# Optimization experiments

Measured on AMD Instinct MI355X. Metric: run time of the kernel, lower is better.

## Reference

```python
import jax, jax.numpy as jnp
import numpy as np
from jax import lax

DG = 8  # deformable groups


def conv3(x, w, b):
    # 3x3 stride-1 SAME conv, NCHW/OIHW
    y = lax.conv_general_dilated(x, w, (1, 1), 'SAME',
                                 dimension_numbers=('NCHW', 'OIHW', 'NCHW'))
    return y + b[None, :, None, None]


def lrelu(x):
    return jnp.where(x >= 0, x, 0.1 * x)


def _mdcn(x, offset, mask, w, b, dg):
    """Modulated deformable conv v2: 3x3, stride 1, pad 1, dilation 1, groups 1.
    offset: [B, 2*dg*9, H, W] (first dg*9 = y offsets, second dg*9 = x offsets),
    mask:   [B, dg*9, H, W] (already sigmoided)."""
    B, C, H, W = x.shape
    kk = 9
    Cg = C // dg
    off = offset.reshape(B, 2, dg, kk, H, W)
    oy, ox = off[:, 0], off[:, 1]            # [B, dg, kk, H, W]
    m = mask.reshape(B, dg, kk, H, W)
    ky = (jnp.arange(kk) // 3 - 1).astype(x.dtype).reshape(1, 1, kk, 1, 1)
    kx = (jnp.arange(kk) % 3 - 1).astype(x.dtype).reshape(1, 1, kk, 1, 1)
    hg = jnp.arange(H, dtype=x.dtype).reshape(1, 1, 1, H, 1)
    wg = jnp.arange(W, dtype=x.dtype).reshape(1, 1, 1, 1, W)
    py = hg + ky + oy                        # sampling positions (pad=1 cancels k-1 shift)
    px = wg + kx + ox
    y0 = jnp.floor(py)
    x0 = jnp.floor(px)
    wy = py - y0
    wx = px - x0
    xg = x.reshape(B, dg, Cg, H * W)
    acc = jnp.zeros((B, dg, Cg, kk, H, W), x.dtype)
    for dy, dx, wgt in ((0.0, 0.0, (1 - wy) * (1 - wx)),
                        (0.0, 1.0, (1 - wy) * wx),
                        (1.0, 0.0, wy * (1 - wx)),
                        (1.0, 1.0, wy * wx)):
        yy = y0 + dy
        xx = x0 + dx
        valid = (yy >= 0) & (yy < H) & (xx >= 0) & (xx < W)
        yi = jnp.clip(yy, 0, H - 1).astype(jnp.int32)
        xi = jnp.clip(xx, 0, W - 1).astype(jnp.int32)
        idx = (yi * W + xi).reshape(B, dg, 1, kk * H * W)
        v = jnp.take_along_axis(xg, idx, axis=3).reshape(B, dg, Cg, kk, H, W)
        acc = acc + v * (wgt * valid.astype(x.dtype))[:, :, None]
    acc = acc * m[:, :, None]                # modulation mask
    sampled = acc.reshape(B, C, kk, H, W)
    out = jnp.einsum('bckhw,ock->bohw', sampled, w.reshape(w.shape[0], C, kk))
    return out + b[None, :, None, None]


def _dcn_pack(x, feat, w_om, b_om, w, b):
    out = conv3(feat, w_om, b_om)            # [B, 3*dg*9, H, W]
    o1, o2, mr = jnp.split(out, 3, axis=1)
    offset = jnp.concatenate([o1, o2], axis=1)
    mask = jax.nn.sigmoid(mr)
    return _mdcn(x, offset, mask, w, b, DG)


def _forward(ref, neb,
             w_oc1, b_oc1, w_om1, b_om1, w_dcn1, b_dcn1, w_fc, b_fc,
             w_cas1, b_cas1, w_cas2, b_cas2, w_om2, b_om2, w_dcn2, b_dcn2,
             w_ta1, b_ta1, w_ta2, b_ta2, w_ff, b_ff):
    start = ref
    # --- PCD alignment (nbr_feat_l = neb, ref_feat_l = ref) ---
    off = lrelu(conv3(jnp.concatenate([neb, ref], axis=1), w_oc1, b_oc1))
    feat = _dcn_pack(neb, off, w_om1, b_om1, w_dcn1, b_dcn1)
    feat = lrelu(conv3(feat, w_fc, b_fc))
    off = jnp.concatenate([feat, ref], axis=1)
    off = lrelu(conv3(lrelu(conv3(off, w_cas1, b_cas1)), w_cas2, b_cas2))
    feat = lrelu(_dcn_pack(feat, off, w_om2, b_om2, w_dcn2, b_dcn2))
    # --- TSA fusion (ref=ref, neb=feat) ---
    emb_ref = conv3(ref, w_ta1, b_ta1)
    emb = conv3(feat, w_ta2, b_ta2)
    corr = jnp.sum(emb * emb_ref, axis=1, keepdims=True)  # [B,1,H,W]
    feat = lrelu(conv3(ref * corr, w_ff, b_ff))
    return feat + start


def setup_inputs() -> dict:
    key = jax.random.key(0)
    ks = jax.random.split(key, 32)
    B, C, H, W = 4, 64, 180, 320
    s = 0.05
    p = lambda k, shape: (jax.random.normal(k, shape, jnp.float32) * s)
    OM = 3 * DG * 9  # 216
    return {
        'ref': jax.random.normal(ks[0], (B, C, H, W), jnp.float32),
        'neb': jax.random.normal(ks[1], (B, C, H, W), jnp.float32),
        'w_oc1': p(ks[2], (C, 2 * C, 3, 3)), 'b_oc1': p(ks[3], (C,)),
        'w_om1': p(ks[4], (OM, C, 3, 3)),    'b_om1': p(ks[5], (OM,)),
        'w_dcn1': p(ks[6], (C, C, 3, 3)),    'b_dcn1': p(ks[7], (C,)),
        'w_fc': p(ks[8], (C, C, 3, 3)),      'b_fc': p(ks[9], (C,)),
        'w_cas1': p(ks[10], (C, 2 * C, 3, 3)), 'b_cas1': p(ks[11], (C,)),
        'w_cas2': p(ks[12], (C, C, 3, 3)),   'b_cas2': p(ks[13], (C,)),
        'w_om2': p(ks[14], (OM, C, 3, 3)),   'b_om2': p(ks[15], (OM,)),
        'w_dcn2': p(ks[16], (C, C, 3, 3)),   'b_dcn2': p(ks[17], (C,)),
        'w_ta1': p(ks[18], (C, C, 3, 3)),    'b_ta1': p(ks[19], (C,)),
        'w_ta2': p(ks[20], (C, C, 3, 3)),    'b_ta2': p(ks[21], (C,)),
        'w_ff': p(ks[22], (C, C, 3, 3)),     'b_ff': p(ks[23], (C,)),
    }


def reference(ref, neb,
              w_oc1, b_oc1, w_om1, b_om1, w_dcn1, b_dcn1, w_fc, b_fc,
              w_cas1, b_cas1, w_cas2, b_cas2, w_om2, b_om2, w_dcn2, b_dcn2,
              w_ta1, b_ta1, w_ta2, b_ta2, w_ff, b_ff):
    return _forward(ref, neb,
                    w_oc1, b_oc1, w_om1, b_om1, w_dcn1, b_dcn1, w_fc, b_fc,
                    w_cas1, b_cas1, w_cas2, b_cas2, w_om2, b_om2, w_dcn2, b_dcn2,
                    w_ta1, b_ta1, w_ta2, b_ta2, w_ff, b_ff)
```

## Files before the change

kernel.cpp:

```cpp
#include <hip/hip_runtime.h>
#include <cmath>


using short8 = __attribute__((ext_vector_type(8))) short;
using f32x4  = __attribute__((ext_vector_type(4))) float;

#define DEVINL static __device__ __forceinline__

DEVINL unsigned short f2bf(float f){
    unsigned u = __float_as_uint(f);
    u += 0x7fffu + ((u >> 16) & 1u);
    return (unsigned short)(u >> 16);
}
DEVINL unsigned pack2(float a, float b){ return (unsigned)f2bf(a) | ((unsigned)f2bf(b) << 16); }
DEVINL float bflo(unsigned u){ return __uint_as_float(u << 16); }
DEVINL float bfhi(unsigned u){ return __uint_as_float(u & 0xffff0000u); }
DEVINL float bf2f(unsigned short u){ return __uint_as_float((unsigned)u << 16); }
DEVINL float lrelu_f(float v){ return v >= 0.f ? v : 0.1f * v; }

__global__ __launch_bounds__(256) void nchw2nhwc2(const float* __restrict__ inA,
                                                  const float* __restrict__ inB,
                                                  unsigned short* __restrict__ outA,
                                                  unsigned short* __restrict__ outB)
{
    constexpr int HW = 180 * 320;
    const int blk = blockIdx.x;
    const float* in = (blk < 900) ? inA : inB;
    unsigned short* out = (blk < 900) ? outA : outB;
    size_t idx = (size_t)(blk % 900) * 256 + threadIdx.x;
    size_t bb = idx / HW, p = idx % HW;
    const float* src = in + (bb * 64) * (size_t)HW + p;
    unsigned short* dst = out + idx * 64;
    #pragma unroll
    for (int c0 = 0; c0 < 64; c0 += 16) {
        unsigned r[8];
        #pragma unroll
        for (int q = 0; q < 8; ++q)
            r[q] = pack2(src[(size_t)(c0 + 2*q) * HW], src[(size_t)(c0 + 2*q + 1) * HW]);
        *(uint4*)(dst + c0)     = *(uint4*)&r[0];
        *(uint4*)(dst + c0 + 8) = *(uint4*)&r[4];
    }
}

struct PrepArgs {
    const float* src[11];
    unsigned short* dst[11];
    int cout[11]; int cin[11]; int nch[11]; int kind[11];
};

__global__ __launch_bounds__(256) void prep_all(PrepArgs a)
{
    const int t = blockIdx.y;
    const int idx = blockIdx.x * 256 + threadIdx.x;
    if (a.kind[t] == 1) {
        if (idx >= 36864) return;
        int kk = idx & 31, oc = (idx >> 5) & 63, s = idx >> 11;
        int k = s * 32 + kk;
        int gt = k >> 3, c8 = k & 7;
        int g = gt / 9, tp = gt - g * 9;
        a.dst[t][idx] = f2bf(a.src[t][((size_t)oc * 64 + g * 8 + c8) * 9 + tp]);
    } else {
        int cin = a.cin[t], cout = a.cout[t];
        int ncs = cin / 32;
        int total = a.nch[t] * 9 * ncs * 2048;
        if (idx >= total) return;
        int kk = idx & 31, oc_l = (idx >> 5) & 63, rest = idx >> 11;
        int cs = rest % ncs; int rest2 = rest / ncs;
        int j = rest2 % 9; int ch = rest2 / 9;
        int oc = ch * 64 + oc_l, c = cs * 32 + kk;
        float v = (oc < cout) ? a.src[t][((size_t)oc * cin + c) * 9 + j] : 0.f;
        a.dst[t][idx] = f2bf(v);
    }
}

template<int CIN, bool TWO_IN, bool ACT, bool SCALE, int OUTMODE>
__global__ __launch_bounds__(256, (CIN == 128 ? 2 : 3)) void conv_mfma(
    const unsigned short* __restrict__ in0, const unsigned short* __restrict__ in1,
    const unsigned short* __restrict__ wgt, const float* __restrict__ bias,
    unsigned short* __restrict__ out, const float* __restrict__ corr,
    const float* __restrict__ res, float* __restrict__ outf, int COUT)
{
    constexpr int H = 180, W = 320, HW = H * W;
    constexpr int NCB = CIN / 8;
    constexpr int NCS = CIN / 32;
    __shared__ __align__(16) unsigned char lds[6 * 34 * CIN * 2];

    const int tid = threadIdx.x;
    const int b  = (OUTMODE == 1) ? 0 : blockIdx.z;
    const int ch = (OUTMODE == 1) ? blockIdx.z : 0;
    const int x0 = blockIdx.x * 32, y0 = blockIdx.y * 4;

    for (int t = tid; t < 6 * 34 * NCB; t += 256) {
        int cb = t % NCB; int r = t / NCB;
        int xp = r % 34, yp = r / 34;
        int gx = x0 - 1 + xp, gy = y0 - 1 + yp;
        uint4 v = make_uint4(0, 0, 0, 0);
        if (gx >= 0 && gx < W && gy >= 0 && gy < H) {
            size_t pix = (size_t)b * HW + (size_t)gy * W + gx;
            const unsigned short* src;
            if (TWO_IN) src = (cb < 8) ? (in0 + pix * 64 + cb * 8) : (in1 + pix * 64 + (cb - 8) * 8);
            else        src = in0 + pix * CIN + cb * 8;
            v = *(const uint4*)src;
            if (SCALE) {
                float cv = corr[pix];
                v.x = pack2(bflo(v.x) * cv, bfhi(v.x) * cv);
                v.y = pack2(bflo(v.y) * cv, bfhi(v.y) * cv);
                v.z = pack2(bflo(v.z) * cv, bfhi(v.z) * cv);
                v.w = pack2(bflo(v.w) * cv, bfhi(v.w) * cv);
            }
        }
        int blk = cb ^ (xp & 7);
        *(uint4*)&lds[(size_t)((yp * 34 + xp) * NCB + blk) * 16] = v;
    }
    __syncthreads();

    const int wv = tid >> 6, lane = tid & 63;
    const int ll = lane & 15, lh = lane >> 4;
    const unsigned short* wchunk = wgt + (size_t)ch * (9 * NCS * 2048);
    const int alane = ll * 32 + lh * 8;

    f32x4 acc[4][2];
    #pragma unroll
    for (int mi = 0; mi < 4; ++mi)
        #pragma unroll
        for (int nf = 0; nf < 2; ++nf) acc[mi][nf] = f32x4{0.f, 0.f, 0.f, 0.f};

    #pragma unroll
    for (int j = 0; j < 9; ++j) {
        const int jy = j / 3, jx = j % 3;
        #pragma unroll
        for (int cs = 0; cs < NCS; ++cs) {
            const int s = j * NCS + cs;
            short8 a[4];
            #pragma unroll
            for (int mi = 0; mi < 4; ++mi)
                a[mi] = *(const short8*)(wchunk + (size_t)s * 2048 + mi * 512 + alane);
            short8 bf[2];
            #pragma unroll
            for (int nf = 0; nf < 2; ++nf) {
                int xp = nf * 16 + ll + jx;
                int blk = (cs * 4 + lh) ^ (xp & 7);
                int addr = (((wv + jy) * 34 + xp) * NCB + blk) * 16;
                bf[nf] = *(const short8*)&lds[addr];
            }
            #pragma unroll
            for (int mi = 0; mi < 4; ++mi)
                #pragma unroll
                for (int nf = 0; nf < 2; ++nf)
                    acc[mi][nf] = __builtin_amdgcn_mfma_f32_16x16x32_bf16(a[mi], bf[nf], acc[mi][nf], 0, 0, 0);
        }
    }

    const int py = y0 + wv;
    const size_t pixrow = (size_t)b * HW + (size_t)py * W;
    #pragma unroll
    for (int nf = 0; nf < 2; ++nf) {
        const int px = x0 + nf * 16 + ll;
        if (OUTMODE == 3) {
            float dot = 0.f;
            const unsigned* er = (const unsigned*)(in1 + (pixrow + px) * 64);
            #pragma unroll
            for (int mi = 0; mi < 4; ++mi) {
                const int oc_l = mi * 16 + lh * 4;
                unsigned e0 = er[oc_l / 2], e1 = er[oc_l / 2 + 1];
                float t0 = acc[mi][nf][0] + bias[oc_l + 0];
                float t1 = acc[mi][nf][1] + bias[oc_l + 1];
                float t2 = acc[mi][nf][2] + bias[oc_l + 2];
                float t3 = acc[mi][nf][3] + bias[oc_l + 3];
                dot += t0 * bflo(e0) + t1 * bfhi(e0) + t2 * bflo(e1) + t3 * bfhi(e1);
            }
            dot += __shfl_xor(dot, 16);
            dot += __shfl_xor(dot, 32);
            if (lh == 0) outf[pixrow + px] = dot;
        } else {
            #pragma unroll
            for (int mi = 0; mi < 4; ++mi) {
                const int oc_l = mi * 16 + lh * 4;
                if (OUTMODE == 0) {
                    float v[4];
                    #pragma unroll
                    for (int jj = 0; jj < 4; ++jj) {
                        float t = acc[mi][nf][jj] + bias[oc_l + jj];
                        v[jj] = ACT ? lrelu_f(t) : t;
                    }
                    uint2 st; st.x = pack2(v[0], v[1]); st.y = pack2(v[2], v[3]);
                    *(uint2*)&out[(pixrow + px) * 64 + oc_l] = st;
                } else if (OUTMODE == 1) {
                    #pragma unroll
                    for (int jj = 0; jj < 4; ++jj) {
                        int ocg = ch * 64 + oc_l + jj;
                        if (ocg < COUT) {
                            float t = acc[mi][nf][jj] + bias[ocg];
                            out[(size_t)ocg * HW + (size_t)py * W + px] = f2bf(ACT ? lrelu_f(t) : t);
                        }
                    }
                } else {
                    #pragma unroll
                    for (int jj = 0; jj < 4; ++jj) {
                        int oc = oc_l + jj;
                        float t = acc[mi][nf][jj] + bias[oc];
                        if (ACT) t = lrelu_f(t);
                        size_t idx = ((size_t)b * 64 + oc) * HW + (size_t)py * W + px;
                        outf[idx] = t + res[idx];
                    }
                }
            }
        }
    }
}

template<int ACT>
__global__ __launch_bounds__(256, 4) void mdcn_mfma(
    const unsigned short* __restrict__ x, size_t xstride,
    const unsigned short* __restrict__ om, size_t omstride,
    const unsigned short* __restrict__ wgt, const float* __restrict__ bias,
    unsigned short* __restrict__ out, size_t ostride)
{
    constexpr int H = 180, W = 320, HW = H * W;
    __shared__ __align__(16) unsigned char sv[72 * 32 * 16];

    const int tid = threadIdx.x;
    const unsigned short* xb  = x  + (size_t)blockIdx.z * xstride;
    const unsigned short* omb = om + (size_t)blockIdx.z * omstride;
    unsigned short* ob        = out + (size_t)blockIdx.z * ostride;
    const int px0 = blockIdx.x * 32;
    const int py  = blockIdx.y;

    {
        const int pxl = tid & 31, g = tid >> 5;
        const int px = px0 + pxl;
        const size_t p = (size_t)py * W + px;
        const unsigned short* omg = omb + (size_t)(g * 9) * HW + p;

        float oyv[9], oxv[9], mmv[9];
        #pragma unroll
        for (int k = 0; k < 9; ++k) oyv[k] = bf2f(omg[(size_t)k * HW]);
        #pragma unroll
        for (int k = 0; k < 9; ++k) oxv[k] = bf2f(omg[(size_t)(72 + k) * HW]);
        #pragma unroll
        for (int k = 0; k < 9; ++k) mmv[k] = bf2f(omg[(size_t)(144 + k) * HW]);

        #pragma unroll
        for (int k = 0; k < 9; ++k) {
            float m = 1.f / (1.f + __expf(-mmv[k]));
            float pyf = (float)(py + (k / 3) - 1) + oyv[k];
            float pxf = (float)(px + (k % 3) - 1) + oxv[k];
            float y0f = floorf(pyf), x0f = floorf(pxf);
            float wy = pyf - y0f, wx = pxf - x0f;
            int yi = (int)y0f, xi = (int)x0f;
            bool vy0 = (yi >= 0) && (yi < H);
            bool vy1 = (yi + 1 >= 0) && (yi + 1 < H);
            bool vx0 = (xi >= 0) && (xi < W);
            bool vx1 = (xi + 1 >= 0) && (xi + 1 < W);
            float w00 = (vy0 && vx0) ? (1.f - wy) * (1.f - wx) * m : 0.f;
            float w01 = (vy0 && vx1) ? (1.f - wy) * wx * m : 0.f;
            float w10 = (vy1 && vx0) ? wy * (1.f - wx) * m : 0.f;
            float w11 = (vy1 && vx1) ? wy * wx * m : 0.f;
            int yc0 = min(max(yi, 0), H - 1), yc1 = min(max(yi + 1, 0), H - 1);
            int xc0 = min(max(xi, 0), W - 1), xc1 = min(max(xi + 1, 0), W - 1);
            uint4 c00 = *(const uint4*)(xb + ((size_t)(yc0 * W + xc0) * 64 + g * 8));
            uint4 c01 = *(const uint4*)(xb + ((size_t)(yc0 * W + xc1) * 64 + g * 8));
            uint4 c10 = *(const uint4*)(xb + ((size_t)(yc1 * W + xc0) * 64 + g * 8));
            uint4 c11 = *(const uint4*)(xb + ((size_t)(yc1 * W + xc1) * 64 + g * 8));
            const unsigned* p00 = (const unsigned*)&c00;
            const unsigned* p01 = (const unsigned*)&c01;
            const unsigned* p10 = (const unsigned*)&c10;
            const unsigned* p11 = (const unsigned*)&c11;
            unsigned r[4];
            #pragma unroll
            for (int q = 0; q < 4; ++q) {
                float lo = w00 * bflo(p00[q]) + w01 * bflo(p01[q]) + w10 * bflo(p10[q]) + w11 * bflo(p11[q]);
                float hi = w00 * bfhi(p00[q]) + w01 * bfhi(p01[q]) + w10 * bfhi(p10[q]) + w11 * bfhi(p11[q]);
                r[q] = pack2(lo, hi);
            }
            *(uint4*)&sv[(size_t)((g * 9 + k) * 32 + pxl) * 16] = *(uint4*)r;
        }
    }
    __syncthreads();

    const int wv = tid >> 6, lane = tid & 63;
    const int ll = lane & 15, lh = lane >> 4;
    f32x4 acc[2] = {f32x4{0.f,0.f,0.f,0.f}, f32x4{0.f,0.f,0.f,0.f}};
    #pragma unroll
    for (int s = 0; s < 18; ++s) {
        short8 a = *(const short8*)(wgt + (size_t)(s * 64 + wv * 16 + ll) * 32 + lh * 8);
        #pragma unroll
        for (int nf = 0; nf < 2; ++nf) {
            short8 bb = *(const short8*)&sv[(size_t)s * 2048 + lh * 512 + (nf * 16 + ll) * 16];
            acc[nf] = __builtin_amdgcn_mfma_f32_16x16x32_bf16(a, bb, acc[nf], 0, 0, 0);
        }
    }
    #pragma unroll
    for (int nf = 0; nf < 2; ++nf) {
        int opx = px0 + nf * 16 + ll;
        int oc0 = wv * 16 + lh * 4;
        float v[4];
        #pragma unroll
        for (int jj = 0; jj < 4; ++jj) {
            float t = acc[nf][jj] + bias[oc0 + jj];
            v[jj] = ACT ? lrelu_f(t) : t;
        }
        uint2 st; st.x = pack2(v[0], v[1]); st.y = pack2(v[2], v[3]);
        *(uint2*)&ob[((size_t)py * W + opx) * 64 + oc0] = st;
    }
}

extern "C" void kernel_launch(void* const* d_in, const int* in_sizes, int n_in,
                              void* d_out, int out_size, void* d_ws, size_t ws_size,
                              hipStream_t stream)
{
    const float* ref    = (const float*)d_in[0];
    const float* neb    = (const float*)d_in[1];
    const float* w_oc1  = (const float*)d_in[2];  const float* b_oc1  = (const float*)d_in[3];
    const float* w_om1  = (const float*)d_in[4];  const float* b_om1  = (const float*)d_in[5];
    const float* w_dcn1 = (const float*)d_in[6];  const float* b_dcn1 = (const float*)d_in[7];
    const float* w_fc   = (const float*)d_in[8];  const float* b_fc   = (const float*)d_in[9];
    const float* w_cas1 = (const float*)d_in[10]; const float* b_cas1 = (const float*)d_in[11];
    const float* w_cas2 = (const float*)d_in[12]; const float* b_cas2 = (const float*)d_in[13];
    const float* w_om2  = (const float*)d_in[14]; const float* b_om2  = (const float*)d_in[15];
    const float* w_dcn2 = (const float*)d_in[16]; const float* b_dcn2 = (const float*)d_in[17];
    const float* w_ta1  = (const float*)d_in[18]; const float* b_ta1  = (const float*)d_in[19];
    const float* w_ta2  = (const float*)d_in[20]; const float* b_ta2  = (const float*)d_in[21];
    const float* w_ff   = (const float*)d_in[22]; const float* b_ff   = (const float*)d_in[23];

    constexpr int H = 180, W = 320, HW = H * W;
    constexpr size_t CHW = (size_t)HW * 64;
    constexpr size_t SLB = 4 * CHW * 2;
    constexpr size_t OMSLOT_EL = (size_t)HW * 216;
    constexpr size_t OMSLOT_B  = OMSLOT_EL * 2;

    char* wsb = (char*)d_ws;
    unsigned short* S0 = (unsigned short*)(wsb);
    unsigned short* S1 = (unsigned short*)(wsb + SLB);
    unsigned short* S2 = (unsigned short*)(wsb + 2 * SLB);
    unsigned short* S3 = (unsigned short*)(wsb + 3 * SLB);
    float* corrf = (float*)S3;
    unsigned short* ffw = (unsigned short*)(wsb + SLB + (2u << 20));

    char* doutb = (char*)d_out;
    unsigned short* omA0 = (unsigned short*)doutb;
    unsigned short* omA1 = omA0 + OMSLOT_EL;
    unsigned short* wb   = (unsigned short*)(doutb + 2 * OMSLOT_B);
    const bool big = ws_size >= 4 * SLB + 2 * OMSLOT_B;
    unsigned short* omB0 = (unsigned short*)(wsb + 4 * SLB);
    unsigned short* omB1 = omB0 + OMSLOT_EL;

    unsigned short* w_oc1p = wb + 0;
    unsigned short* w_om1p = wb + 73728;
    unsigned short* w_dcn1p= wb + 221184;
    unsigned short* w_fcp  = wb + 258048;
    unsigned short* w_cas1p= wb + 294912;
    unsigned short* w_cas2p= wb + 368640;
    unsigned short* w_om2p = wb + 405504;
    unsigned short* w_dcn2p= wb + 552960;
    unsigned short* w_ta1p = wb + 589824;
    unsigned short* w_ta2p = wb + 626688;
    unsigned short* w_ffp  = wb + 663552;

    dim3 blk(256);
    dim3 g4(10, 45, 4);
    dim3 gm(10, 180, 2);

    nchw2nhwc2<<<1800, blk, 0, stream>>>(ref, neb, S0, S1);

    {
        PrepArgs pa;
        const float* srcs[11] = {w_oc1, w_om1, w_dcn1, w_fc, w_cas1, w_cas2, w_om2, w_dcn2, w_ta1, w_ta2, w_ff};
        unsigned short* dsts[11] = {w_oc1p, w_om1p, w_dcn1p, w_fcp, w_cas1p, w_cas2p, w_om2p, w_dcn2p, w_ta1p, w_ta2p, w_ffp};
        int couts[11] = {64, 216, 0, 64, 64, 64, 216, 0, 64, 64, 64};
        int cins[11]  = {128, 64, 0, 64, 128, 64, 64, 0, 64, 64, 64};
        int nchs[11]  = {1, 4, 0, 1, 1, 1, 4, 0, 1, 1, 1};
        int kinds[11] = {0, 0, 1, 0, 0, 0, 0, 1, 0, 0, 0};
        for (int i = 0; i < 11; ++i) {
            pa.src[i] = srcs[i]; pa.dst[i] = dsts[i];
            pa.cout[i] = couts[i]; pa.cin[i] = cins[i]; pa.nch[i] = nchs[i]; pa.kind[i] = kinds[i];
        }
        prep_all<<<dim3(576, 11), blk, 0, stream>>>(pa);
    }

    conv_mfma<128, true, true, false, 0><<<g4, blk, 0, stream>>>(
        S1, S0, w_oc1p, b_oc1, S2, nullptr, nullptr, nullptr, 64);

    auto omconv = [&](const unsigned short* inp, const unsigned short* wp, const float* bp,
                      unsigned short* slot){
        conv_mfma<64, false, false, false, 1><<<g4, blk, 0, stream>>>(
            inp, nullptr, wp, bp, slot, nullptr, nullptr, nullptr, 216);
    };

    if (big) {
        omconv(S2 + 0 * CHW, w_om1p, b_om1, omA0);
        omconv(S2 + 1 * CHW, w_om1p, b_om1, omA1);
        omconv(S2 + 2 * CHW, w_om1p, b_om1, omB0);
        omconv(S2 + 3 * CHW, w_om1p, b_om1, omB1);
        mdcn_mfma<0><<<gm, blk, 0, stream>>>(S1, CHW, omA0, OMSLOT_EL, w_dcn1p, b_dcn1, S3, CHW);
        mdcn_mfma<0><<<gm, blk, 0, stream>>>(S1 + 2 * CHW, CHW, omB0, OMSLOT_EL, w_dcn1p, b_dcn1, S3 + 2 * CHW, CHW);
    } else {
        for (int pp = 0; pp < 2; ++pp) {
            omconv(S2 + (2 * pp) * CHW, w_om1p, b_om1, omA0);
            omconv(S2 + (2 * pp + 1) * CHW, w_om1p, b_om1, omA1);
            mdcn_mfma<0><<<gm, blk, 0, stream>>>(S1 + 2 * pp * CHW, CHW, omA0, OMSLOT_EL,
                                                 w_dcn1p, b_dcn1, S3 + 2 * pp * CHW, CHW);
        }
    }

    conv_mfma<64, false, true, false, 0><<<g4, blk, 0, stream>>>(
        S3, nullptr, w_fcp, b_fc, S2, nullptr, nullptr, nullptr, 64);
    conv_mfma<128, true, true, false, 0><<<g4, blk, 0, stream>>>(
        S2, S0, w_cas1p, b_cas1, S1, nullptr, nullptr, nullptr, 64);
    conv_mfma<64, false, true, false, 0><<<g4, blk, 0, stream>>>(
        S1, nullptr, w_cas2p, b_cas2, S3, nullptr, nullptr, nullptr, 64);

    if (big) {
        omconv(S3 + 0 * CHW, w_om2p, b_om2, omA0);
        omconv(S3 + 1 * CHW, w_om2p, b_om2, omA1);
        omconv(S3 + 2 * CHW, w_om2p, b_om2, omB0);
        omconv(S3 + 3 * CHW, w_om2p, b_om2, omB1);
        mdcn_mfma<1><<<gm, blk, 0, stream>>>(S2, CHW, omA0, OMSLOT_EL, w_dcn2p, b_dcn2, S1, CHW);
        mdcn_mfma<1><<<gm, blk, 0, stream>>>(S2 + 2 * CHW, CHW, omB0, OMSLOT_EL, w_dcn2p, b_dcn2, S1 + 2 * CHW, CHW);
    } else {
        for (int pp = 0; pp < 2; ++pp) {
            omconv(S3 + (2 * pp) * CHW, w_om2p, b_om2, omA0);
            omconv(S3 + (2 * pp + 1) * CHW, w_om2p, b_om2, omA1);
            mdcn_mfma<1><<<gm, blk, 0, stream>>>(S2 + 2 * pp * CHW, CHW, omA0, OMSLOT_EL,
                                                 w_dcn2p, b_dcn2, S1 + 2 * pp * CHW, CHW);
        }
    }

    conv_mfma<64, false, false, false, 0><<<g4, blk, 0, stream>>>(
        S0, nullptr, w_ta1p, b_ta1, S2, nullptr, nullptr, nullptr, 64);
    conv_mfma<64, false, false, false, 3><<<g4, blk, 0, stream>>>(
        S1, S2, w_ta2p, b_ta2, nullptr, nullptr, nullptr, corrf, 64);

    hipMemcpyAsync(ffw, w_ffp, 36864 * 2, hipMemcpyDeviceToDevice, stream);

    conv_mfma<64, false, true, true, 2><<<g4, blk, 0, stream>>>(
        S0, nullptr, ffw, b_ff, nullptr, corrf, ref, (float*)d_out, 64);
}
```

Baseline: 1.295 ms.

## Batch offset/mask convs into two launches, trim padded channel chunk, add XCD swizzle

New measurement: 1.185 ms. 8.5% less time.

```diff
diff --git a/kernel.cpp b/kernel.cpp
--- a/kernel.cpp
+++ b/kernel.cpp
@@ -17,6 +17,20 @@
 DEVINL float bfhi(unsigned u){ return __uint_as_float(u & 0xffff0000u); }
 DEVINL float bf2f(unsigned short u){ return __uint_as_float((unsigned)u << 16); }
 DEVINL float lrelu_f(float v){ return v >= 0.f ? v : 0.1f * v; }
+
+DEVINL void swz_decode(int& bx, int& by, int& bz){
+    const int gx = gridDim.x, gy = gridDim.y;
+    int lin = blockIdx.x + gx * (blockIdx.y + gy * blockIdx.z);
+    int nwg = gx * gy * gridDim.z;
+    int q = nwg >> 3, r = nwg & 7;
+    int xcd = lin & 7, idx = lin >> 3;
+    int swz = (xcd < r ? xcd * (q + 1) : r + xcd * q) + idx;
+    bz = swz / (gx * gy);
+    int rem = swz - bz * gx * gy;
+    by = rem / gx; bx = rem - by * gx;
+}
+
+struct Ptr4 { unsigned short* p[4]; };
 
 __global__ __launch_bounds__(256) void nchw2nhwc2(const float* __restrict__ inA,
                                                   const float* __restrict__ inB,
@@ -73,12 +87,13 @@
     }
 }
 
-template<int CIN, bool TWO_IN, bool ACT, bool SCALE, int OUTMODE>
+template<int CIN, bool TWO_IN, bool ACT, bool SCALE, int OUTMODE, int NM>
 __global__ __launch_bounds__(256, (CIN == 128 ? 2 : 3)) void conv_mfma(
     const unsigned short* __restrict__ in0, const unsigned short* __restrict__ in1,
     const unsigned short* __restrict__ wgt, const float* __restrict__ bias,
     unsigned short* __restrict__ out, const float* __restrict__ corr,
-    const float* __restrict__ res, float* __restrict__ outf, int COUT)
+    const float* __restrict__ res, float* __restrict__ outf,
+    Ptr4 omout, int choff, int zdiv, int COUT)
 {
     constexpr int H = 180, W = 320, HW = H * W;
     constexpr int NCB = CIN / 8;
@@ -86,9 +101,12 @@
     __shared__ __align__(16) unsigned char lds[6 * 34 * CIN * 2];
 
     const int tid = threadIdx.x;
-    const int b  = (OUTMODE == 1) ? 0 : blockIdx.z;
-    const int ch = (OUTMODE == 1) ? blockIdx.z : 0;
-    const int x0 = blockIdx.x * 32, y0 = blockIdx.y * 4;
+    int bx, by, bz;
+    swz_decode(bx, by, bz);
+    int b, ch;
+    if (OUTMODE == 1) { b = bz / zdiv; ch = bz % zdiv + choff; }
+    else              { b = bz; ch = 0; }
+    const int x0 = bx * 32, y0 = by * 4;
 
     for (int t = tid; t < 6 * 34 * NCB; t += 256) {
         int cb = t % NCB; int r = t / NCB;
@@ -119,9 +137,9 @@
     const unsigned short* wchunk = wgt + (size_t)ch * (9 * NCS * 2048);
     const int alane = ll * 32 + lh * 8;
 
-    f32x4 acc[4][2];
-    #pragma unroll
-    for (int mi = 0; mi < 4; ++mi)
+    f32x4 acc[NM][2];
+    #pragma unroll
+    for (int mi = 0; mi < NM; ++mi)
         #pragma unroll
         for (int nf = 0; nf < 2; ++nf) acc[mi][nf] = f32x4{0.f, 0.f, 0.f, 0.f};
 
@@ -131,9 +149,9 @@
         #pragma unroll
         for (int cs = 0; cs < NCS; ++cs) {
             const int s = j * NCS + cs;
-            short8 a[4];
-            #pragma unroll
-            for (int mi = 0; mi < 4; ++mi)
+            short8 a[NM];
+            #pragma unroll
+            for (int mi = 0; mi < NM; ++mi)
                 a[mi] = *(const short8*)(wchunk + (size_t)s * 2048 + mi * 512 + alane);
             short8 bf[2];
             #pragma unroll
@@ -144,7 +162,7 @@
                 bf[nf] = *(const short8*)&lds[addr];
             }
             #pragma unroll
-            for (int mi = 0; mi < 4; ++mi)
+            for (int mi = 0; mi < NM; ++mi)
                 #pragma unroll
                 for (int nf = 0; nf < 2; ++nf)
                     acc[mi][nf] = __builtin_amdgcn_mfma_f32_16x16x32_bf16(a[mi], bf[nf], acc[mi][nf], 0, 0, 0);
@@ -160,7 +178,7 @@
             float dot = 0.f;
             const unsigned* er = (const unsigned*)(in1 + (pixrow + px) * 64);
             #pragma unroll
-            for (int mi = 0; mi < 4; ++mi) {
+            for (int mi = 0; mi < NM; ++mi) {
                 const int oc_l = mi * 16 + lh * 4;
                 unsigned e0 = er[oc_l / 2], e1 = er[oc_l / 2 + 1];
                 float t0 = acc[mi][nf][0] + bias[oc_l + 0];
@@ -172,9 +190,23 @@
             dot += __shfl_xor(dot, 16);
             dot += __shfl_xor(dot, 32);
             if (lh == 0) outf[pixrow + px] = dot;
+        } else if (OUTMODE == 1) {
+            unsigned short* oslot = omout.p[b];
+            #pragma unroll
+            for (int mi = 0; mi < NM; ++mi) {
+                const int oc_l = mi * 16 + lh * 4;
+                #pragma unroll
+                for (int jj = 0; jj < 4; ++jj) {
+                    int ocg = ch * 64 + oc_l + jj;
+                    if (ocg < COUT) {
+                        float t = acc[mi][nf][jj] + bias[ocg];
+                        oslot[(size_t)ocg * HW + (size_t)py * W + px] = f2bf(ACT ? lrelu_f(t) : t);
+                    }
+                }
+            }
         } else {
             #pragma unroll
-            for (int mi = 0; mi < 4; ++mi) {
+            for (int mi = 0; mi < NM; ++mi) {
                 const int oc_l = mi * 16 + lh * 4;
                 if (OUTMODE == 0) {
                     float v[4];
@@ -185,15 +217,6 @@
                     }
                     uint2 st; st.x = pack2(v[0], v[1]); st.y = pack2(v[2], v[3]);
                     *(uint2*)&out[(pixrow + px) * 64 + oc_l] = st;
-                } else if (OUTMODE == 1) {
-                    #pragma unroll
-                    for (int jj = 0; jj < 4; ++jj) {
-                        int ocg = ch * 64 + oc_l + jj;
-                        if (ocg < COUT) {
-                            float t = acc[mi][nf][jj] + bias[ocg];
-                            out[(size_t)ocg * HW + (size_t)py * W + px] = f2bf(ACT ? lrelu_f(t) : t);
-                        }
-                    }
                 } else {
                     #pragma unroll
                     for (int jj = 0; jj < 4; ++jj) {
@@ -220,11 +243,13 @@
     __shared__ __align__(16) unsigned char sv[72 * 32 * 16];
 
     const int tid = threadIdx.x;
-    const unsigned short* xb  = x  + (size_t)blockIdx.z * xstride;
-    const unsigned short* omb = om + (size_t)blockIdx.z * omstride;
-    unsigned short* ob        = out + (size_t)blockIdx.z * ostride;
-    const int px0 = blockIdx.x * 32;
-    const int py  = blockIdx.y;
+    int bx, by, bz;
+    swz_decode(bx, by, bz);
+    const unsigned short* xb  = x  + (size_t)bz * xstride;
+    const unsigned short* omb = om + (size_t)bz * omstride;
+    unsigned short* ob        = out + (size_t)bz * ostride;
+    const int px0 = bx * 32;
+    const int py  = by;
 
     {
         const int pxl = tid & 31, g = tid >> 5;
@@ -360,6 +385,7 @@
     dim3 blk(256);
     dim3 g4(10, 45, 4);
     dim3 gm(10, 180, 2);
+    Ptr4 none{};
 
     nchw2nhwc2<<<1800, blk, 0, stream>>>(ref, neb, S0, S1);
 
@@ -378,61 +404,59 @@
         prep_all<<<dim3(576, 11), blk, 0, stream>>>(pa);
     }
 
-    conv_mfma<128, true, true, false, 0><<<g4, blk, 0, stream>>>(
-        S1, S0, w_oc1p, b_oc1, S2, nullptr, nullptr, nullptr, 64);
-
-    auto omconv = [&](const unsigned short* inp, const unsigned short* wp, const float* bp,
-                      unsigned short* slot){
-        conv_mfma<64, false, false, false, 1><<<g4, blk, 0, stream>>>(
-            inp, nullptr, wp, bp, slot, nullptr, nullptr, nullptr, 216);
+    conv_mfma<128, true, true, false, 0, 4><<<g4, blk, 0, stream>>>(
+        S1, S0, w_oc1p, b_oc1, S2, nullptr, nullptr, nullptr, none, 0, 1, 64);
+
+    auto ompack = [&](const unsigned short* inp, const unsigned short* wp, const float* bp,
+                      Ptr4 slots, int nb){
+        conv_mfma<64, false, false, false, 1, 4><<<dim3(10, 45, 3 * nb), blk, 0, stream>>>(
+            inp, nullptr, wp, bp, nullptr, nullptr, nullptr, nullptr, slots, 0, 3, 216);
+        conv_mfma<64, false, false, false, 1, 2><<<dim3(10, 45, nb), blk, 0, stream>>>(
+            inp, nullptr, wp, bp, nullptr, nullptr, nullptr, nullptr, slots, 3, 1, 216);
     };
 
     if (big) {
-        omconv(S2 + 0 * CHW, w_om1p, b_om1, omA0);
-        omconv(S2 + 1 * CHW, w_om1p, b_om1, omA1);
-        omconv(S2 + 2 * CHW, w_om1p, b_om1, omB0);
-        omconv(S2 + 3 * CHW, w_om1p, b_om1, omB1);
+        Ptr4 slots{omA0, omA1, omB0, omB1};
+        ompack(S2, w_om1p, b_om1, slots, 4);
         mdcn_mfma<0><<<gm, blk, 0, stream>>>(S1, CHW, omA0, OMSLOT_EL, w_dcn1p, b_dcn1, S3, CHW);
         mdcn_mfma<0><<<gm, blk, 0, stream>>>(S1 + 2 * CHW, CHW, omB0, OMSLOT_EL, w_dcn1p, b_dcn1, S3 + 2 * CHW, CHW);
     } else {
+        Ptr4 slots{omA0, omA1, nullptr, nullptr};
         for (int pp = 0; pp < 2; ++pp) {
-            omconv(S2 + (2 * pp) * CHW, w_om1p, b_om1, omA0);
-            omconv(S2 + (2 * pp + 1) * CHW, w_om1p, b_om1, omA1);
+            ompack(S2 + 2 * pp * CHW, w_om1p, b_om1, slots, 2);
             mdcn_mfma<0><<<gm, blk, 0, stream>>>(S1 + 2 * pp * CHW, CHW, omA0, OMSLOT_EL,
                                                  w_dcn1p, b_dcn1, S3 + 2 * pp * CHW, CHW);
         }
     }
 
-    conv_mfma<64, false, true, false, 0><<<g4, blk, 0, stream>>>(
-        S3, nullptr, w_fcp, b_fc, S2, nullptr, nullptr, nullptr, 64);
-    conv_mfma<128, true, true, false, 0><<<g4, blk, 0, stream>>>(
-        S2, S0, w_cas1p, b_cas1, S1, nullptr, nullptr, nullptr, 64);
-    conv_mfma<64, false, true, false, 0><<<g4, blk, 0, stream>>>(
-        S1, nullptr, w_cas2p, b_cas2, S3, nullptr, nullptr, nullptr, 64);
+    conv_mfma<64, false, true, false, 0, 4><<<g4, blk, 0, stream>>>(
+        S3, nullptr, w_fcp, b_fc, S2, nullptr, nullptr, nullptr, none, 0, 1, 64);
+    conv_mfma<128, true, true, false, 0, 4><<<g4, blk, 0, stream>>>(
+        S2, S0, w_cas1p, b_cas1, S1, nullptr, nullptr, nullptr, none, 0, 1, 64);
+    conv_mfma<64, false, true, false, 0, 4><<<g4, blk, 0, stream>>>(
+        S1, nullptr, w_cas2p, b_cas2, S3, nullptr, nullptr, nullptr, none, 0, 1, 64);
 
     if (big) {
-        omconv(S3 + 0 * CHW, w_om2p, b_om2, omA0);
-        omconv(S3 + 1 * CHW, w_om2p, b_om2, omA1);
-        omconv(S3 + 2 * CHW, w_om2p, b_om2, omB0);
-        omconv(S3 + 3 * CHW, w_om2p, b_om2, omB1);
+        Ptr4 slots{omA0, omA1, omB0, omB1};
+        ompack(S3, w_om2p, b_om2, slots, 4);
         mdcn_mfma<1><<<gm, blk, 0, stream>>>(S2, CHW, omA0, OMSLOT_EL, w_dcn2p, b_dcn2, S1, CHW);
         mdcn_mfma<1><<<gm, blk, 0, stream>>>(S2 + 2 * CHW, CHW, omB0, OMSLOT_EL, w_dcn2p, b_dcn2, S1 + 2 * CHW, CHW);
     } else {
+        Ptr4 slots{omA0, omA1, nullptr, nullptr};
         for (int pp = 0; pp < 2; ++pp) {
-            omconv(S3 + (2 * pp) * CHW, w_om2p, b_om2, omA0);
-            omconv(S3 + (2 * pp + 1) * CHW, w_om2p, b_om2, omA1);
+            ompack(S3 + 2 * pp * CHW, w_om2p, b_om2, slots, 2);
             mdcn_mfma<1><<<gm, blk, 0, stream>>>(S2 + 2 * pp * CHW, CHW, omA0, OMSLOT_EL,
                                                  w_dcn2p, b_dcn2, S1 + 2 * pp * CHW, CHW);
         }
     }
 
-    conv_mfma<64, false, false, false, 0><<<g4, blk, 0, stream>>>(
-        S0, nullptr, w_ta1p, b_ta1, S2, nullptr, nullptr, nullptr, 64);
-    conv_mfma<64, false, false, false, 3><<<g4, blk, 0, stream>>>(
-        S1, S2, w_ta2p, b_ta2, nullptr, nullptr, nullptr, corrf, 64);
+    conv_mfma<64, false, false, false, 0, 4><<<g4, blk, 0, stream>>>(
+        S0, nullptr, w_ta1p, b_ta1, S2, nullptr, nullptr, nullptr, none, 0, 1, 64);
+    conv_mfma<64, false, false, false, 3, 4><<<g4, blk, 0, stream>>>(
+        S1, S2, w_ta2p, b_ta2, nullptr, nullptr, nullptr, corrf, none, 0, 1, 64);
 
     hipMemcpyAsync(ffw, w_ffp, 36864 * 2, hipMemcpyDeviceToDevice, stream);
 
-    conv_mfma<64, false, true, true, 2><<<g4, blk, 0, stream>>>(
-        S0, nullptr, ffw, b_ff, nullptr, corrf, ref, (float*)d_out, 64);
-}
+    conv_mfma<64, false, true, true, 2, 4><<<g4, blk, 0, stream>>>(
+        S0, nullptr, ffw, b_ff, nullptr, corrf, ref, (float*)d_out, none, 0, 1, 64);
+}
```
